# Kernel optimization log

Measured on AMD Instinct MI355X. Metric: run time of the kernel, lower is better.

Reference implementation:

```python
import jax, jax.numpy as jnp
import numpy as np

D_MODEL = 1024
N_HEADS = 16
D_K = D_MODEL // N_HEADS


def setup_inputs() -> dict:
    key = jax.random.key(0)
    ks = jax.random.split(key, 9)
    s = 0.02
    x = jax.random.normal(ks[0], (2, 2048, D_MODEL), dtype=jnp.float32)
    Wq = jax.random.normal(ks[1], (D_MODEL, D_MODEL), dtype=jnp.float32) * s
    bq = jax.random.normal(ks[2], (D_MODEL,), dtype=jnp.float32) * s
    Wk = jax.random.normal(ks[3], (D_MODEL, D_MODEL), dtype=jnp.float32) * s
    bk = jax.random.normal(ks[4], (D_MODEL,), dtype=jnp.float32) * s
    Wv = jax.random.normal(ks[5], (D_MODEL, D_MODEL), dtype=jnp.float32) * s
    bv = jax.random.normal(ks[6], (D_MODEL,), dtype=jnp.float32) * s
    Wo = jax.random.normal(ks[7], (D_MODEL, D_MODEL), dtype=jnp.float32) * s
    bo = jax.random.normal(ks[8], (D_MODEL,), dtype=jnp.float32) * s
    return {"x": x, "Wq": Wq, "bq": bq, "Wk": Wk, "bk": bk,
            "Wv": Wv, "bv": bv, "Wo": Wo, "bo": bo}


def reference(x, Wq, bq, Wk, bk, Wv, bv, Wo, bo):
    B, S, D = x.shape
    # nn.Linear: y = x @ W.T + b
    q = x @ Wq.T + bq  # [B,S,D]
    k = x @ Wk.T + bk
    v = x @ Wv.T + bv
    # split heads -> [B,H,S,dk]
    q = q.reshape(B, S, N_HEADS, D_K).transpose(0, 2, 1, 3)
    k = k.reshape(B, S, N_HEADS, D_K).transpose(0, 2, 1, 3)
    v = v.reshape(B, S, N_HEADS, D_K).transpose(0, 2, 1, 3)
    scale = 1.0 / jnp.sqrt(jnp.asarray(D_K, dtype=x.dtype))
    scores = jnp.einsum('bhqd,bhkd->bhqk', q, k) * scale  # [B,H,S,S]
    weights = jax.nn.softmax(scores, axis=-1)
    out = jnp.einsum('bhqk,bhkd->bhqd', weights, v)  # [B,H,S,dk]
    concat = out.transpose(0, 2, 1, 3).reshape(B, S, D)
    return concat @ Wo.T + bo
```

## Files before the change

kernel.cpp:

```cpp
#include <hip/hip_runtime.h>

typedef unsigned short ushort_t;
typedef __attribute__((ext_vector_type(8))) __bf16 bf16x8;
typedef __attribute__((ext_vector_type(4))) float floatx4;

#define AS1 __attribute__((address_space(1)))
#define AS3 __attribute__((address_space(3)))

#define D_MODEL 1024
#define NH 16
#define DKH 64
#define SEQ 2048
#define NB 2
#define MTOT (NB * SEQ)

#define QSCALE 0.18033688011112042f

#define OFF_X   0u
#define OFF_WQ  4194304u
#define OFF_BQ  5242880u
#define OFF_WK  5243904u
#define OFF_BK  6292480u
#define OFF_WV  6293504u
#define OFF_BV  7342080u
#define OFF_WO  7343104u
#define OFF_BO  8391680u
#define CVT_TOT 8392704u

__device__ __forceinline__ float bf2f(ushort_t u) {
    union { unsigned u; float f; } v; v.u = ((unsigned)u) << 16; return v.f;
}
__device__ __forceinline__ ushort_t f2bf(float f) {
    union { float f; unsigned u; } v; v.f = f;
    unsigned r = v.u + 0x7FFFu + ((v.u >> 16) & 1u);
    return (ushort_t)(r >> 16);
}
__device__ __forceinline__ unsigned pack2bf(float a, float b) {
    unsigned ua = __float_as_uint(a), ub = __float_as_uint(b);
    ua = ua + 0x7FFFu + ((ua >> 16) & 1u);
    ub = ub + 0x7FFFu + ((ub >> 16) & 1u);
    return __builtin_amdgcn_perm(ub, ua, 0x07060302);
}
__device__ __forceinline__ unsigned cvtpk(float a, float b) {
    unsigned r;
    asm("v_cvt_pk_bf16_f32 %0, %1, %2" : "=v"(r) : "v"(a), "v"(b));
    return r;
}
__device__ __forceinline__ float fexp2(float x) { return __builtin_amdgcn_exp2f(x); }

#define GSYNC(N) do { \
    asm volatile("s_waitcnt vmcnt(" #N ")" ::: "memory"); \
    __builtin_amdgcn_s_barrier(); \
    __builtin_amdgcn_sched_barrier(0); \
} while (0)

__global__ __launch_bounds__(256) void convert_kernel(
    const float* __restrict__ x,  const float* __restrict__ wq, const float* __restrict__ bq_,
    const float* __restrict__ wk, const float* __restrict__ bk_, const float* __restrict__ wv,
    const float* __restrict__ bv_, const float* __restrict__ wo, const float* __restrict__ bo_,
    ushort_t* __restrict__ dst)
{
    const unsigned idx = ((unsigned)blockIdx.x * 256u + threadIdx.x) * 4u;
    if (idx >= CVT_TOT) return;
    const float* src; unsigned off;
    if      (idx < OFF_WQ) { src = x;   off = idx - OFF_X;  }
    else if (idx < OFF_BQ) { src = wq;  off = idx - OFF_WQ; }
    else if (idx < OFF_WK) { src = bq_; off = idx - OFF_BQ; }
    else if (idx < OFF_BK) { src = wk;  off = idx - OFF_WK; }
    else if (idx < OFF_WV) { src = bk_; off = idx - OFF_BK; }
    else if (idx < OFF_BV) { src = wv;  off = idx - OFF_WV; }
    else if (idx < OFF_WO) { src = bv_; off = idx - OFF_BV; }
    else if (idx < OFF_BO) { src = wo;  off = idx - OFF_WO; }
    else                   { src = bo_; off = idx - OFF_BO; }
    float4 v = *reinterpret_cast<const float4*>(src + off);
    uint2 p;
    p.x = pack2bf(v.x, v.y);
    p.y = pack2bf(v.z, v.w);
    *reinterpret_cast<uint2*>(dst + idx) = p;
}

__device__ __forceinline__ void gemm_core_qkv(
    const ushort_t* __restrict__ X, const ushort_t* __restrict__ W,
    int m0, int n0, ushort_t* lds, floatx4 acc[4][4])
{
    const int tid = threadIdx.x;
    const int lane = tid & 63, wv = tid >> 6;
    const int wm = (wv >> 1) * 64, wn = (wv & 1) * 64;
    const int l15 = lane & 15, quad = lane >> 4;
    const floatx4 z4 = {0.f, 0.f, 0.f, 0.f};
#pragma unroll
    for (int i = 0; i < 4; ++i)
#pragma unroll
        for (int j = 0; j < 4; ++j) acc[i][j] = z4;
    const int lrow = lane >> 2;
    const int lcol = (lane & 3) * 8;
    const ushort_t* gA = X + (size_t)(m0 + lrow) * D_MODEL + lcol;
    const ushort_t* gB = W + (size_t)(n0 + lrow) * D_MODEL + lcol;

    auto STAGE = [&](ushort_t* Ln, int k0) {
#pragma unroll
        for (int j = 0; j < 2; ++j) {
            const int rA = (wv * 2 + j) * 16;
            __builtin_amdgcn_global_load_lds(
                (const AS1 unsigned*)(gA + (size_t)rA * D_MODEL + k0),
                (AS3 unsigned*)(Ln + rA * 32), 16, 0, 0);
        }
        const int rB = wv * 16;
        __builtin_amdgcn_global_load_lds(
            (const AS1 unsigned*)(gB + (size_t)rB * D_MODEL + k0),
            (AS3 unsigned*)(Ln + 8192 + rB * 32), 16, 0, 0);
    };
    auto COMPUTE = [&](const ushort_t* L) {
        bf16x8 af[4], bfr[4];
#pragma unroll
        for (int i = 0; i < 4; ++i)
            af[i] = *reinterpret_cast<const bf16x8*>(L + (wm + i * 16 + l15) * 32 + quad * 8);
#pragma unroll
        for (int j = 0; j < 4; ++j)
            bfr[j] = *reinterpret_cast<const bf16x8*>(L + 8192 + (wn + j * 16 + l15) * 32 + quad * 8);
#pragma unroll
        for (int i = 0; i < 4; ++i)
#pragma unroll
            for (int j = 0; j < 4; ++j)
                acc[i][j] = __builtin_amdgcn_mfma_f32_16x16x32_bf16(af[i], bfr[j], acc[i][j], 0, 0, 0);
    };

    ushort_t* b0 = lds;
    ushort_t* b1 = lds + 12288;
    ushort_t* b2 = lds + 24576;
    STAGE(b0, 0);
    STAGE(b1, 32);
    for (int tt = 0; tt < 30; tt += 3) {
        GSYNC(3); STAGE(b2, (tt + 2) * 32); COMPUTE(b0);
        GSYNC(3); STAGE(b0, (tt + 3) * 32); COMPUTE(b1);
        GSYNC(3); STAGE(b1, (tt + 4) * 32); COMPUTE(b2);
    }
    GSYNC(3); COMPUTE(b0);
    GSYNC(0); COMPUTE(b1);
}

__global__ __launch_bounds__(512, 2) void qkv_kernel(
    const ushort_t* __restrict__ x,
    const ushort_t* __restrict__ Wq, const ushort_t* __restrict__ bq,
    const ushort_t* __restrict__ Wk, const ushort_t* __restrict__ bk,
    const ushort_t* __restrict__ Wv, const ushort_t* __restrict__ bv,
    ushort_t* __restrict__ q_ws, ushort_t* __restrict__ k_ws, ushort_t* __restrict__ vt_ws)
{
    __shared__ __align__(16) ushort_t lds[36864];
    const int L = blockIdx.x;
    const int xcd = L & 7;
    const int r = L >> 3;
    const int n_idx = xcd * 3 + (r % 3);
    const int m_idx = r / 3;
    const int m0 = m_idx * 256;
    const int which = n_idx >> 3;
    const int n0 = (n_idx & 7) * 128;
    const ushort_t* W    = (which == 0) ? Wq : (which == 1) ? Wk : Wv;
    const ushort_t* bias = (which == 0) ? bq : (which == 1) ? bk : bv;
    floatx4 acc[4][4];
    gemm_core_qkv(x, W, m0, n0, lds, acc);
    const int tid = threadIdx.x, lane = tid & 63, wv = tid >> 6;
    const int wm = (wv >> 1) * 64, wn = (wv & 1) * 64;
    const int l15 = lane & 15, quad = lane >> 4;
    const int b0 = m0 >> 11;
    const int s0 = m0 & (SEQ - 1);
    __syncthreads();
    if (which < 2) {
        ushort_t* Ts = lds;
        ushort_t* dst = (which == 0) ? q_ws : k_ws;
        const float scl = (which == 0) ? QSCALE : 1.0f;
#pragma unroll
        for (int j = 0; j < 4; ++j) {
            int coln = wn + j * 16 + l15;
            float bb = bf2f(bias[n0 + coln]);
#pragma unroll
            for (int i = 0; i < 4; ++i)
#pragma unroll
                for (int rr = 0; rr < 4; ++rr) {
                    int rowm = wm + i * 16 + quad * 4 + rr;
                    Ts[rowm * 136 + coln] = f2bf((acc[i][j][rr] + bb) * scl);
                }
        }
        __syncthreads();
#pragma unroll
        for (int i = 0; i < 8; ++i) {
            int c = tid + 512 * i;
            int rowm = c >> 4, chunk = c & 15;
            float4 v = *reinterpret_cast<const float4*>(Ts + rowm * 136 + chunk * 8);
            int s = s0 + rowm;
            int n = n0 + chunk * 8, h = n >> 6, d = n & 63;
            *reinterpret_cast<float4*>(dst + (((size_t)(b0 * NH + h)) * SEQ + s) * DKH + d) = v;
        }
    } else {
        ushort_t* Ts = lds;
#pragma unroll
        for (int j = 0; j < 4; ++j) {
            int coln = wn + j * 16 + l15;
            float bb = bf2f(bias[n0 + coln]);
#pragma unroll
            for (int i = 0; i < 4; ++i)
#pragma unroll
                for (int rr = 0; rr < 4; ++rr) {
                    int rowm = wm + i * 16 + quad * 4 + rr;
                    Ts[coln * 264 + rowm] = f2bf(acc[i][j][rr] + bb);
                }
        }
        __syncthreads();
#pragma unroll
        for (int i = 0; i < 8; ++i) {
            int c = tid + 512 * i;
            int nr = c >> 5, mc = (c & 31) * 8;
            float4 v = *reinterpret_cast<const float4*>(Ts + nr * 264 + mc);
            int n = n0 + nr, h = n >> 6, d = n & 63;
            *reinterpret_cast<float4*>(vt_ws + (((size_t)(b0 * NH + h)) * DKH + d) * SEQ + s0 + mc) = v;
        }
    }
}

__global__ __launch_bounds__(512, 4) void attn_kernel(
    const ushort_t* __restrict__ q_ws, const ushort_t* __restrict__ k_ws,
    const ushort_t* __restrict__ vt_ws, ushort_t* __restrict__ concat)
{
    __shared__ __align__(16) ushort_t sm[36864];
    const int L = blockIdx.x;
    const int qb = (L >> 3) & 15;
    const int bh = (L & 7) + ((L >> 7) << 3);
    const int tid = threadIdx.x;
    const int lane = tid & 63, wv = tid >> 6;
    const int half = wv >> 2, wq = wv & 3;
    const int l15 = lane & 15, quad = lane >> 4;
    const int ht = tid & 255;

    const ushort_t* Qg = q_ws + ((size_t)bh * SEQ + qb * 128) * DKH;
    const ushort_t* Kg = k_ws + ((size_t)bh * SEQ + half * (SEQ / 2)) * DKH;
    const ushort_t* Vg = vt_ws + (size_t)bh * DKH * SEQ + half * (SEQ / 2);

    ushort_t* Ks     = sm + half * 4608;
    ushort_t* VTs    = sm + 9216 + half * 4608;
    ushort_t* Ps     = sm + 18432 + wv * 2304;
    ushort_t* Qstage = sm + 18432;

    const int r0c = ht >> 3,         c0c = (ht & 7) * 8;
    const int r1c = (ht + 256) >> 3, c1c = ((ht + 256) & 7) * 8;

#pragma unroll
    for (int i = 0; i < 2; ++i) {
        int c = tid + 512 * i;
        int row = c >> 3, col = (c & 7) * 8;
        *reinterpret_cast<float4*>(Qstage + row * 72 + col) =
            *reinterpret_cast<const float4*>(Qg + row * DKH + col);
    }
    __syncthreads();
    bf16x8 aq[2][2];
#pragma unroll
    for (int nt = 0; nt < 2; ++nt)
#pragma unroll
        for (int ks = 0; ks < 2; ++ks)
            aq[nt][ks] = *reinterpret_cast<const bf16x8*>(Qstage + (wq * 32 + nt * 16 + l15) * 72 + ks * 32 + quad * 8);

    const floatx4 z4 = {0.f, 0.f, 0.f, 0.f};
    floatx4 o[2][4];
    floatx4 la4[2] = {z4, z4};
#pragma unroll
    for (int nt = 0; nt < 2; ++nt)
#pragma unroll
        for (int dt = 0; dt < 4; ++dt) o[nt][dt] = z4;

    float4 pk0 = *reinterpret_cast<const float4*>(Kg + (size_t)r0c * DKH + c0c);
    float4 pk1 = *reinterpret_cast<const float4*>(Kg + (size_t)r1c * DKH + c1c);
    float4 pv0 = *reinterpret_cast<const float4*>(Vg + (size_t)r0c * SEQ + c0c);
    float4 pv1 = *reinterpret_cast<const float4*>(Vg + (size_t)r1c * SEQ + c1c);

    for (int t = 0; t < 16; ++t) {
        __syncthreads();
        *reinterpret_cast<float4*>(Ks + r0c * 72 + c0c) = pk0;
        *reinterpret_cast<float4*>(Ks + r1c * 72 + c1c) = pk1;
        *reinterpret_cast<float4*>(VTs + r0c * 72 + c0c) = pv0;
        *reinterpret_cast<float4*>(VTs + r1c * 72 + c1c) = pv1;
        __syncthreads();
        if (t < 15) {
            int toff = (t + 1) * 64;
            pk0 = *reinterpret_cast<const float4*>(Kg + (size_t)(toff + r0c) * DKH + c0c);
            pk1 = *reinterpret_cast<const float4*>(Kg + (size_t)(toff + r1c) * DKH + c1c);
            pv0 = *reinterpret_cast<const float4*>(Vg + (size_t)r0c * SEQ + toff + c0c);
            pv1 = *reinterpret_cast<const float4*>(Vg + (size_t)r1c * SEQ + toff + c1c);
        }

        floatx4 st[2][4];
        __builtin_amdgcn_s_setprio(1);
#pragma unroll
        for (int mt = 0; mt < 4; ++mt) {
            bf16x8 akf = *reinterpret_cast<const bf16x8*>(Ks + (mt * 16 + l15) * 72 + quad * 8);
            st[0][mt] = __builtin_amdgcn_mfma_f32_16x16x32_bf16(akf, aq[0][0], z4, 0, 0, 0);
            st[1][mt] = __builtin_amdgcn_mfma_f32_16x16x32_bf16(akf, aq[1][0], z4, 0, 0, 0);
        }
#pragma unroll
        for (int mt = 0; mt < 4; ++mt) {
            bf16x8 akf = *reinterpret_cast<const bf16x8*>(Ks + (mt * 16 + l15) * 72 + 32 + quad * 8);
            st[0][mt] = __builtin_amdgcn_mfma_f32_16x16x32_bf16(akf, aq[0][1], st[0][mt], 0, 0, 0);
            st[1][mt] = __builtin_amdgcn_mfma_f32_16x16x32_bf16(akf, aq[1][1], st[1][mt], 0, 0, 0);
        }
        __builtin_amdgcn_s_setprio(0);

#pragma unroll
        for (int nt = 0; nt < 2; ++nt)
#pragma unroll
            for (int mt = 0; mt < 4; ++mt) {
#pragma unroll
                for (int rr = 0; rr < 4; ++rr) st[nt][mt][rr] = fexp2(st[nt][mt][rr]);
                la4[nt] += st[nt][mt];
                uint2 pk;
                pk.x = cvtpk(st[nt][mt][0], st[nt][mt][1]);
                pk.y = cvtpk(st[nt][mt][2], st[nt][mt][3]);
                *reinterpret_cast<uint2*>(Ps + (nt * 16 + l15) * 72 + mt * 16 + quad * 4) = pk;
            }
        asm volatile("s_waitcnt lgkmcnt(0)" ::: "memory");
        __builtin_amdgcn_s_setprio(1);
#pragma unroll
        for (int ks = 0; ks < 2; ++ks) {
            bf16x8 ap0 = *reinterpret_cast<const bf16x8*>(Ps + l15 * 72 + ks * 32 + quad * 8);
            bf16x8 ap1 = *reinterpret_cast<const bf16x8*>(Ps + (16 + l15) * 72 + ks * 32 + quad * 8);
#pragma unroll
            for (int dt = 0; dt < 4; ++dt) {
                bf16x8 bvv = *reinterpret_cast<const bf16x8*>(VTs + (dt * 16 + l15) * 72 + ks * 32 + quad * 8);
                o[0][dt] = __builtin_amdgcn_mfma_f32_16x16x32_bf16(ap0, bvv, o[0][dt], 0, 0, 0);
                o[1][dt] = __builtin_amdgcn_mfma_f32_16x16x32_bf16(ap1, bvv, o[1][dt], 0, 0, 0);
            }
        }
        __builtin_amdgcn_s_setprio(0);
    }
    float lsum[2];
#pragma unroll
    for (int nt = 0; nt < 2; ++nt) {
        float s = la4[nt][0] + la4[nt][1] + la4[nt][2] + la4[nt][3];
        s += __shfl_xor(s, 16, 64);
        s += __shfl_xor(s, 32, 64);
        lsum[nt] = s;
    }
    __syncthreads();
    float* Of = (float*)sm;
    float* lf = Of + 128 * 68;
    if (half == 1) {
#pragma unroll
        for (int nt = 0; nt < 2; ++nt) {
            if (quad == 0) lf[wq * 32 + nt * 16 + l15] = lsum[nt];
#pragma unroll
            for (int rr = 0; rr < 4; ++rr) {
                int row = wq * 32 + nt * 16 + quad * 4 + rr;
#pragma unroll
                for (int dt = 0; dt < 4; ++dt)
                    Of[row * 68 + dt * 16 + l15] = o[nt][dt][rr];
            }
        }
    }
    __syncthreads();
    if (half == 0) {
        const int b0 = bh >> 4, h = bh & 15;
#pragma unroll
        for (int nt = 0; nt < 2; ++nt) {
            float ltot = lsum[nt] + lf[wq * 32 + nt * 16 + l15];
            float linv = 1.f / ltot;
#pragma unroll
            for (int rr = 0; rr < 4; ++rr) {
                float lB = __shfl(linv, quad * 4 + rr, 64);
                int row = wq * 32 + nt * 16 + quad * 4 + rr;
                size_t base = ((size_t)(b0 * SEQ + qb * 128 + row)) * D_MODEL + h * DKH;
#pragma unroll
                for (int dt = 0; dt < 4; ++dt) {
                    float sum = o[nt][dt][rr] + Of[row * 68 + dt * 16 + l15];
                    concat[base + dt * 16 + l15] = f2bf(sum * lB);
                }
            }
        }
    }
}

__global__ __launch_bounds__(512, 2) void oproj_kernel(
    const ushort_t* __restrict__ cc, const ushort_t* __restrict__ Wo,
    const ushort_t* __restrict__ bo, float* __restrict__ out)
{
    __shared__ __align__(16) ushort_t lds[24576];
    const int L = blockIdx.x;
    const int n0 = (L & 7) * 128;
    const int m0 = (L >> 3) * 128;
    const int tid = threadIdx.x;
    const int lane = tid & 63, wv = tid >> 6;
    const int wm = (wv >> 2) * 64, wn = (wv & 3) * 32;
    const int l15 = lane & 15, quad = lane >> 4;
    const floatx4 z4 = {0.f, 0.f, 0.f, 0.f};
    floatx4 acc[4][2];
#pragma unroll
    for (int i = 0; i < 4; ++i)
#pragma unroll
        for (int j = 0; j < 2; ++j) acc[i][j] = z4;
    const int lrow = lane >> 2;
    const int lcol = (lane & 3) * 8;
    const ushort_t* gA = cc + (size_t)(m0 + lrow) * D_MODEL + lcol;
    const ushort_t* gB = Wo + (size_t)(n0 + lrow) * D_MODEL + lcol;

    auto STAGE = [&](ushort_t* Ln, int k0) {
        const int r0 = wv * 16;
        __builtin_amdgcn_global_load_lds(
            (const AS1 unsigned*)(gA + (size_t)r0 * D_MODEL + k0),
            (AS3 unsigned*)(Ln + r0 * 32), 16, 0, 0);
        __builtin_amdgcn_global_load_lds(
            (const AS1 unsigned*)(gB + (size_t)r0 * D_MODEL + k0),
            (AS3 unsigned*)(Ln + 4096 + r0 * 32), 16, 0, 0);
    };
    auto COMPUTE = [&](const ushort_t* Lb) {
        bf16x8 af[4], bfr[2];
#pragma unroll
        for (int i = 0; i < 4; ++i)
            af[i] = *reinterpret_cast<const bf16x8*>(Lb + (wm + i * 16 + l15) * 32 + quad * 8);
#pragma unroll
        for (int j = 0; j < 2; ++j)
            bfr[j] = *reinterpret_cast<const bf16x8*>(Lb + 4096 + (wn + j * 16 + l15) * 32 + quad * 8);
#pragma unroll
        for (int i = 0; i < 4; ++i)
#pragma unroll
            for (int j = 0; j < 2; ++j)
                acc[i][j] = __builtin_amdgcn_mfma_f32_16x16x32_bf16(af[i], bfr[j], acc[i][j], 0, 0, 0);
    };

    ushort_t* b0 = lds;
    ushort_t* b1 = lds + 8192;
    ushort_t* b2 = lds + 16384;
    STAGE(b0, 0);
    STAGE(b1, 32);
    for (int tt = 0; tt < 30; tt += 3) {
        GSYNC(2); STAGE(b2, (tt + 2) * 32); COMPUTE(b0);
        GSYNC(2); STAGE(b0, (tt + 3) * 32); COMPUTE(b1);
        GSYNC(2); STAGE(b1, (tt + 4) * 32); COMPUTE(b2);
    }
    GSYNC(2); COMPUTE(b0);
    GSYNC(0); COMPUTE(b1);

#pragma unroll
    for (int j = 0; j < 2; ++j) {
        int n = n0 + wn + j * 16 + l15;
        float bb = bf2f(bo[n]);
#pragma unroll
        for (int i = 0; i < 4; ++i)
#pragma unroll
            for (int rr = 0; rr < 4; ++rr) {
                int m = m0 + wm + i * 16 + quad * 4 + rr;
                out[(size_t)m * D_MODEL + n] = acc[i][j][rr] + bb;
            }
    }
}

extern "C" void kernel_launch(void* const* d_in, const int* in_sizes, int n_in,
                              void* d_out, int out_size, void* d_ws, size_t ws_size,
                              hipStream_t stream)
{
    ushort_t* cvt = (ushort_t*)d_ws;
    const ushort_t* xb  = cvt + OFF_X;
    const ushort_t* Wqb = cvt + OFF_WQ;
    const ushort_t* bqb = cvt + OFF_BQ;
    const ushort_t* Wkb = cvt + OFF_WK;
    const ushort_t* bkb = cvt + OFF_BK;
    const ushort_t* Wvb = cvt + OFF_WV;
    const ushort_t* bvb = cvt + OFF_BV;
    const ushort_t* Wob = cvt + OFF_WO;
    const ushort_t* bob = cvt + OFF_BO;
    ushort_t* q_ws   = cvt + CVT_TOT;
    ushort_t* k_ws   = q_ws  + (size_t)MTOT * D_MODEL;
    ushort_t* vt_ws  = k_ws  + (size_t)MTOT * D_MODEL;
    ushort_t* concat = vt_ws + (size_t)MTOT * D_MODEL;

    convert_kernel<<<(CVT_TOT / 1024), 256, 0, stream>>>(
        (const float*)d_in[0], (const float*)d_in[1], (const float*)d_in[2],
        (const float*)d_in[3], (const float*)d_in[4], (const float*)d_in[5],
        (const float*)d_in[6], (const float*)d_in[7], (const float*)d_in[8], cvt);
    qkv_kernel<<<dim3(384), 512, 0, stream>>>(xb, Wqb, bqb, Wkb, bkb, Wvb, bvb, q_ws, k_ws, vt_ws);
    attn_kernel<<<dim3(512), 512, 0, stream>>>(q_ws, k_ws, vt_ws, concat);
    oproj_kernel<<<dim3(256), 512, 0, stream>>>(concat, Wob, bob, (float*)d_out);
}
```

Baseline: 183.0 us.

## Switch attention kernel MFMAs from 16x16x32 to 32x32x16 tiles

Rewrites the QK^T and PV matrix products in the attention kernel to use 32x32x16 bf16 MFMA instructions with 16-element accumulators instead of 16x16x32 ones. The fragment layouts for Q, K, P and V^T, the P staging writes, the row-sum reduction and the final cross-half combine and normalisation are all remapped to match. The aim is fewer MFMA issues and fewer LDS fragment reads per tile, since the larger instruction gives more reuse per operand load. The trade-offs are more live accumulator registers and different LDS access patterns, which may cause bank conflicts.

```diff
diff --git a/kernel.cpp b/kernel.cpp
--- a/kernel.cpp
+++ b/kernel.cpp
@@ -3,6 +3,7 @@
 typedef unsigned short ushort_t;
 typedef __attribute__((ext_vector_type(8))) __bf16 bf16x8;
 typedef __attribute__((ext_vector_type(4))) float floatx4;
+typedef __attribute__((ext_vector_type(16))) float floatx16;
 
 #define AS1 __attribute__((address_space(1)))
 #define AS3 __attribute__((address_space(3)))
@@ -228,7 +229,7 @@
     const int tid = threadIdx.x;
     const int lane = tid & 63, wv = tid >> 6;
     const int half = wv >> 2, wq = wv & 3;
-    const int l15 = lane & 15, quad = lane >> 4;
+    const int l31 = lane & 31, lh = lane >> 5;
     const int ht = tid & 255;
 
     const ushort_t* Qg = q_ws + ((size_t)bh * SEQ + qb * 128) * DKH;
@@ -251,20 +252,16 @@
             *reinterpret_cast<const float4*>(Qg + row * DKH + col);
     }
     __syncthreads();
-    bf16x8 aq[2][2];
-#pragma unroll
-    for (int nt = 0; nt < 2; ++nt)
-#pragma unroll
-        for (int ks = 0; ks < 2; ++ks)
-            aq[nt][ks] = *reinterpret_cast<const bf16x8*>(Qstage + (wq * 32 + nt * 16 + l15) * 72 + ks * 32 + quad * 8);
-
+    bf16x8 aq[4];
+#pragma unroll
+    for (int d0 = 0; d0 < 4; ++d0)
+        aq[d0] = *reinterpret_cast<const bf16x8*>(Qstage + (wq * 32 + l31) * 72 + d0 * 16 + lh * 8);
+
+    const floatx16 z16 = {0.f,0.f,0.f,0.f, 0.f,0.f,0.f,0.f, 0.f,0.f,0.f,0.f, 0.f,0.f,0.f,0.f};
     const floatx4 z4 = {0.f, 0.f, 0.f, 0.f};
-    floatx4 o[2][4];
-    floatx4 la4[2] = {z4, z4};
-#pragma unroll
-    for (int nt = 0; nt < 2; ++nt)
-#pragma unroll
-        for (int dt = 0; dt < 4; ++dt) o[nt][dt] = z4;
+    floatx16 o[2];
+    o[0] = z16; o[1] = z16;
+    floatx4 la4 = z4;
 
     float4 pk0 = *reinterpret_cast<const float4*>(Kg + (size_t)r0c * DKH + c0c);
     float4 pk1 = *reinterpret_cast<const float4*>(Kg + (size_t)r1c * DKH + c1c);
@@ -286,90 +283,79 @@
             pv1 = *reinterpret_cast<const float4*>(Vg + (size_t)r1c * SEQ + toff + c1c);
         }
 
-        floatx4 st[2][4];
+        floatx16 st[2];
         __builtin_amdgcn_s_setprio(1);
 #pragma unroll
-        for (int mt = 0; mt < 4; ++mt) {
-            bf16x8 akf = *reinterpret_cast<const bf16x8*>(Ks + (mt * 16 + l15) * 72 + quad * 8);
-            st[0][mt] = __builtin_amdgcn_mfma_f32_16x16x32_bf16(akf, aq[0][0], z4, 0, 0, 0);
-            st[1][mt] = __builtin_amdgcn_mfma_f32_16x16x32_bf16(akf, aq[1][0], z4, 0, 0, 0);
-        }
-#pragma unroll
-        for (int mt = 0; mt < 4; ++mt) {
-            bf16x8 akf = *reinterpret_cast<const bf16x8*>(Ks + (mt * 16 + l15) * 72 + 32 + quad * 8);
-            st[0][mt] = __builtin_amdgcn_mfma_f32_16x16x32_bf16(akf, aq[0][1], st[0][mt], 0, 0, 0);
-            st[1][mt] = __builtin_amdgcn_mfma_f32_16x16x32_bf16(akf, aq[1][1], st[1][mt], 0, 0, 0);
+        for (int kt = 0; kt < 2; ++kt) {
+#pragma unroll
+            for (int d0 = 0; d0 < 4; ++d0) {
+                bf16x8 akf = *reinterpret_cast<const bf16x8*>(
+                    Ks + (kt * 32 + l31) * 72 + d0 * 16 + lh * 8);
+                st[kt] = __builtin_amdgcn_mfma_f32_32x32x16_bf16(
+                    akf, aq[d0], (d0 == 0) ? z16 : st[kt], 0, 0, 0);
+            }
         }
         __builtin_amdgcn_s_setprio(0);
 
 #pragma unroll
-        for (int nt = 0; nt < 2; ++nt)
-#pragma unroll
-            for (int mt = 0; mt < 4; ++mt) {
-#pragma unroll
-                for (int rr = 0; rr < 4; ++rr) st[nt][mt][rr] = fexp2(st[nt][mt][rr]);
-                la4[nt] += st[nt][mt];
+        for (int kt = 0; kt < 2; ++kt)
+#pragma unroll
+            for (int g = 0; g < 4; ++g) {
+                st[kt][g*4+0] = fexp2(st[kt][g*4+0]);
+                st[kt][g*4+1] = fexp2(st[kt][g*4+1]);
+                st[kt][g*4+2] = fexp2(st[kt][g*4+2]);
+                st[kt][g*4+3] = fexp2(st[kt][g*4+3]);
+                la4[0] += st[kt][g*4+0];
+                la4[1] += st[kt][g*4+1];
+                la4[2] += st[kt][g*4+2];
+                la4[3] += st[kt][g*4+3];
                 uint2 pk;
-                pk.x = cvtpk(st[nt][mt][0], st[nt][mt][1]);
-                pk.y = cvtpk(st[nt][mt][2], st[nt][mt][3]);
-                *reinterpret_cast<uint2*>(Ps + (nt * 16 + l15) * 72 + mt * 16 + quad * 4) = pk;
+                pk.x = cvtpk(st[kt][g*4+0], st[kt][g*4+1]);
+                pk.y = cvtpk(st[kt][g*4+2], st[kt][g*4+3]);
+                *reinterpret_cast<uint2*>(Ps + l31 * 72 + kt * 32 + g * 8 + 4 * lh) = pk;
             }
         asm volatile("s_waitcnt lgkmcnt(0)" ::: "memory");
         __builtin_amdgcn_s_setprio(1);
 #pragma unroll
-        for (int ks = 0; ks < 2; ++ks) {
-            bf16x8 ap0 = *reinterpret_cast<const bf16x8*>(Ps + l15 * 72 + ks * 32 + quad * 8);
-            bf16x8 ap1 = *reinterpret_cast<const bf16x8*>(Ps + (16 + l15) * 72 + ks * 32 + quad * 8);
-#pragma unroll
-            for (int dt = 0; dt < 4; ++dt) {
-                bf16x8 bvv = *reinterpret_cast<const bf16x8*>(VTs + (dt * 16 + l15) * 72 + ks * 32 + quad * 8);
-                o[0][dt] = __builtin_amdgcn_mfma_f32_16x16x32_bf16(ap0, bvv, o[0][dt], 0, 0, 0);
-                o[1][dt] = __builtin_amdgcn_mfma_f32_16x16x32_bf16(ap1, bvv, o[1][dt], 0, 0, 0);
+        for (int ks = 0; ks < 4; ++ks) {
+            bf16x8 ap = *reinterpret_cast<const bf16x8*>(Ps + l31 * 72 + ks * 16 + lh * 8);
+#pragma unroll
+            for (int dt = 0; dt < 2; ++dt) {
+                bf16x8 bvv = *reinterpret_cast<const bf16x8*>(
+                    VTs + (dt * 32 + l31) * 72 + ks * 16 + lh * 8);
+                o[dt] = __builtin_amdgcn_mfma_f32_32x32x16_bf16(ap, bvv, o[dt], 0, 0, 0);
             }
         }
         __builtin_amdgcn_s_setprio(0);
     }
-    float lsum[2];
-#pragma unroll
-    for (int nt = 0; nt < 2; ++nt) {
-        float s = la4[nt][0] + la4[nt][1] + la4[nt][2] + la4[nt][3];
-        s += __shfl_xor(s, 16, 64);
-        s += __shfl_xor(s, 32, 64);
-        lsum[nt] = s;
-    }
+    float lsum = la4[0] + la4[1] + la4[2] + la4[3];
+    lsum += __shfl_xor(lsum, 32, 64);
+
     __syncthreads();
     float* Of = (float*)sm;
     float* lf = Of + 128 * 68;
+    if (lane < 32) lf[half * 128 + wq * 32 + lane] = lsum;
     if (half == 1) {
 #pragma unroll
-        for (int nt = 0; nt < 2; ++nt) {
-            if (quad == 0) lf[wq * 32 + nt * 16 + l15] = lsum[nt];
-#pragma unroll
-            for (int rr = 0; rr < 4; ++rr) {
-                int row = wq * 32 + nt * 16 + quad * 4 + rr;
-#pragma unroll
-                for (int dt = 0; dt < 4; ++dt)
-                    Of[row * 68 + dt * 16 + l15] = o[nt][dt][rr];
-            }
-        }
+        for (int dt = 0; dt < 2; ++dt)
+#pragma unroll
+            for (int r = 0; r < 16; ++r) {
+                int row = wq * 32 + (r & 3) + 8 * (r >> 2) + 4 * lh;
+                Of[row * 68 + dt * 32 + l31] = o[dt][r];
+            }
     }
     __syncthreads();
     if (half == 0) {
         const int b0 = bh >> 4, h = bh & 15;
 #pragma unroll
-        for (int nt = 0; nt < 2; ++nt) {
-            float ltot = lsum[nt] + lf[wq * 32 + nt * 16 + l15];
-            float linv = 1.f / ltot;
-#pragma unroll
-            for (int rr = 0; rr < 4; ++rr) {
-                float lB = __shfl(linv, quad * 4 + rr, 64);
-                int row = wq * 32 + nt * 16 + quad * 4 + rr;
-                size_t base = ((size_t)(b0 * SEQ + qb * 128 + row)) * D_MODEL + h * DKH;
-#pragma unroll
-                for (int dt = 0; dt < 4; ++dt) {
-                    float sum = o[nt][dt][rr] + Of[row * 68 + dt * 16 + l15];
-                    concat[base + dt * 16 + l15] = f2bf(sum * lB);
-                }
+        for (int r = 0; r < 16; ++r) {
+            int row = wq * 32 + (r & 3) + 8 * (r >> 2) + 4 * lh;
+            float linv = 1.f / (lf[row] + lf[128 + row]);
+            size_t base = ((size_t)(b0 * SEQ + qb * 128 + row)) * D_MODEL + h * DKH;
+#pragma unroll
+            for (int dt = 0; dt < 2; ++dt) {
+                float sum = o[dt][r] + Of[row * 68 + dt * 32 + l31];
+                concat[base + dt * 32 + l31] = f2bf(sum * linv);
             }
         }
     }
```

Result: faster. 179.2 us (-2.1%).
